# Kernel optimization log

Hardware: AMD Instinct MI355X
Metric: run time of the kernel (lower is better)

Reference implementation:

```python
import math
import jax, jax.numpy as jnp
import numpy as np

INPUT_SIZE = 256
HIDDEN_SIZE = 512
HISTORY_SIZE = 2048
SEQ_LEN = 512
BATCH = 256


def setup_inputs() -> dict:
    key = jax.random.key(0)
    ks = jax.random.split(key, 7)
    s = 0.05
    return {
        "x": jax.random.normal(ks[0], (SEQ_LEN, BATCH, INPUT_SIZE), jnp.float32),
        "hidden": jax.random.normal(ks[1], (1, BATCH, HIDDEN_SIZE), jnp.float32),
        "external": jax.random.normal(ks[2], (HISTORY_SIZE, INPUT_SIZE), jnp.float32),
        # GRU params (bias=False): weight_ih [3H, D_in], weight_hh [3H, H]
        "w_ih": jax.random.normal(ks[3], (3 * HIDDEN_SIZE, INPUT_SIZE), jnp.float32) * s,
        "w_hh": jax.random.normal(ks[4], (3 * HIDDEN_SIZE, HIDDEN_SIZE), jnp.float32) * s,
        "w_alpha": jax.random.normal(ks[5], (HISTORY_SIZE, HIDDEN_SIZE), jnp.float32) * s,
        "w_sigma": jax.random.normal(ks[6], (INPUT_SIZE, HIDDEN_SIZE), jnp.float32) * s,
    }


def reference(x, hidden, external, w_ih, w_hh, w_alpha, w_sigma):
    # --- GRU over the sequence (torch gate order: r, z, n) ---
    def gru_step(h, xt):
        gi = xt @ w_ih.T          # [B, 3H]
        gh = h @ w_hh.T           # [B, 3H]
        i_r, i_z, i_n = jnp.split(gi, 3, axis=-1)
        h_r, h_z, h_n = jnp.split(gh, 3, axis=-1)
        r = jax.nn.sigmoid(i_r + h_r)
        z = jax.nn.sigmoid(i_z + h_z)
        n = jnp.tanh(i_n + r * h_n)
        h_new = (1.0 - z) * n + z * h
        return h_new, None

    h_final, _ = jax.lax.scan(gru_step, hidden[0], x)   # [B, H]
    h_final = h_final[None]                              # [1, B, H]

    # Attention weights over history entries and predicted scale
    alpha = jax.nn.softmax(h_final @ w_alpha.T, axis=-1)  # [1, B, history]
    sigma = jnp.exp(h_final @ w_sigma.T)                  # [1, B, D]
    mu = alpha @ external                                 # [1, B, D]

    # Gaussian log-prob with diagonal factor L = diag(sigma) (M = L L^T)
    diff = x - mu                                         # [S, B, D]
    maha = jnp.sum(jnp.square(diff / sigma), axis=-1)     # [S, B]
    log_det = jnp.sum(jnp.log(jnp.abs(sigma)), axis=-1)   # [1, B]
    D = x.shape[-1]
    log2pi = np.float32(np.log(2.0 * np.pi))
    return -0.5 * (maha + D * log2pi) - log_det           # [S, B]
```

## Files before the change

kernel.cpp:

```cpp
#include <hip/hip_runtime.h>
#include <math.h>

#define BATCH 256
#define HID   512
#define DIN   256
#define SEQ   512
#define HIST  2048
#define NBLK  256
#define NGRP  8
#define GB    32

typedef __attribute__((ext_vector_type(8))) short short8;
typedef __attribute__((ext_vector_type(4))) float floatx4;
typedef __attribute__((ext_vector_type(8))) float floatx8;
typedef unsigned long long ull;
typedef unsigned int uint;

__device__ __forceinline__ unsigned short f32_bf16_rtne(float f) {
    uint u = __builtin_bit_cast(uint, f);
    uint r = u + 0x7FFFu + ((u >> 16) & 1u);
    return (unsigned short)(r >> 16);
}
__device__ __forceinline__ float bf16_f32(unsigned short s) {
    uint u = ((uint)s) << 16;
    return __builtin_bit_cast(float, u);
}
__device__ __forceinline__ float sigmoidf_(float v) {
    return 1.0f / (1.0f + __expf(-v));
}

__device__ __forceinline__ int h_widx(int b_local, int u) {
    return ((u >> 5) * 2 + (b_local >> 4)) * 512 +
           ((u >> 3) & 3) * 128 + (b_local & 15) * 8 + (u & 7);
}

__device__ __forceinline__ void lds_barrier() {
    __builtin_amdgcn_sched_barrier(0);
    asm volatile("s_waitcnt lgkmcnt(0)" ::: "memory");
    __builtin_amdgcn_s_barrier();
    __builtin_amdgcn_sched_barrier(0);
}

__global__ __launch_bounds__(256) void split_kernel(
    const float* __restrict__ src, short* __restrict__ hi, short* __restrict__ lo, int n)
{
    int i = blockIdx.x * 256 + threadIdx.x;
    if (i < n) {
        float v = src[i];
        unsigned short h = f32_bf16_rtne(v);
        hi[i] = (short)h;
        lo[i] = (short)f32_bf16_rtne(v - bf16_f32(h));
    }
}

__global__ __launch_bounds__(256) void pack_h_init(
    const float* __restrict__ hidden, uint* __restrict__ hp0)
{
    int i = blockIdx.x * 256 + threadIdx.x;
    int b = i >> 9, u = i & 511;
    int g = b >> 5, bl = b & 31;
    float v = hidden[i];
    unsigned short hi = f32_bf16_rtne(v);
    unsigned short lo = f32_bf16_rtne(v - bf16_f32(hi));
    lo = (unsigned short)(lo & 0xFFFCu);
    hp0[(size_t)g * 16384 + h_widx(bl, u)] = (uint)hi | ((uint)lo << 16);
}

__global__ __launch_bounds__(512, 2) void gru_persistent(
    const float* __restrict__ x,
    const float* __restrict__ hidden,
    uint* __restrict__ hpA, uint* __restrict__ hpB,
    const short* __restrict__ wih_hi, const short* __restrict__ wih_lo,
    const short* __restrict__ whh_hi, const short* __restrict__ whh_lo)
{
    const int bid  = blockIdx.x;
    const int g    = bid & 7;
    const int ublk = bid >> 3;
    const int u0   = ublk * 16;
    const int tid  = threadIdx.x;
    const int w    = tid >> 6;
    const int lane = tid & 63;
    const int quad = lane >> 4;
    const int n16  = lane & 15;
    const int mbase = g * GB;

    short8 Bh[3][3], Bl[3][3];
    #pragma unroll
    for (int gt = 0; gt < 3; ++gt) {
        const int row = gt * HID + u0 + n16;
        Bh[gt][0] = *(const short8*)(wih_hi + (size_t)row * DIN + w * 32 + quad * 8);
        Bl[gt][0] = *(const short8*)(wih_lo + (size_t)row * DIN + w * 32 + quad * 8);
        #pragma unroll
        for (int s = 0; s < 2; ++s) {
            const int K0h = w * 64 + s * 32;
            Bh[gt][1 + s] = *(const short8*)(whh_hi + (size_t)row * HID + K0h + quad * 8);
            Bl[gt][1 + s] = *(const short8*)(whh_lo + (size_t)row * HID + K0h + quad * 8);
        }
    }

    const int ob = tid >> 4;
    const int ou = tid & 15;
    float hp = hidden[(size_t)(mbase + ob) * HID + (u0 + ou)];
    const int my_widx = h_widx(ob, u0 + ou);

    __shared__ float P8[8][2][4][16][20];

#define MFMA3(AH, AL, BH, BL, ACC)                                        \
    ACC = __builtin_amdgcn_mfma_f32_16x16x32_bf16(AH, BH, ACC, 0, 0, 0);  \
    ACC = __builtin_amdgcn_mfma_f32_16x16x32_bf16(AL, BH, ACC, 0, 0, 0);  \
    ACC = __builtin_amdgcn_mfma_f32_16x16x32_bf16(AH, BL, ACC, 0, 0, 0);

    for (int t = 0; t < SEQ; ++t) {
        const uint* hb = ((t & 1) ? hpB : hpA) + (size_t)g * 16384;
        uint*       hd = ((t & 1) ? hpA : hpB) + (size_t)g * 16384;
        const ull*  hb8 = (const ull*)hb;
        const uint  tg  = (uint)t & 3u;

        const float* xt = x + (size_t)t * BATCH * DIN;
        const floatx8 xv0 = *(const floatx8*)(xt + (size_t)(mbase + n16) * DIN + w * 32 + quad * 8);
        const floatx8 xv1 = *(const floatx8*)(xt + (size_t)(mbase + 16 + n16) * DIN + w * 32 + quad * 8);

        ull hv[2][2][4];
        #pragma unroll
        for (int s = 0; s < 2; ++s)
            #pragma unroll
            for (int mt = 0; mt < 2; ++mt) {
                const ull* base = hb8 + (size_t)(((2 * w + s) * 2 + mt) * 64 + lane) * 4;
                #pragma unroll
                for (int j2 = 0; j2 < 4; ++j2)
                    hv[s][mt][j2] = __hip_atomic_load(base + j2, __ATOMIC_RELAXED,
                                                      __HIP_MEMORY_SCOPE_AGENT);
            }
        __builtin_amdgcn_sched_barrier(0);

        floatx4 acc[2][4];
        #pragma unroll
        for (int mt = 0; mt < 2; ++mt)
            #pragma unroll
            for (int a = 0; a < 4; ++a)
                acc[mt][a] = (floatx4){0.f, 0.f, 0.f, 0.f};

        #pragma unroll
        for (int mt = 0; mt < 2; ++mt) {
            const floatx8 xv = mt ? xv1 : xv0;
            short8 Ah, Al;
            #pragma unroll
            for (int j = 0; j < 8; ++j) {
                const float v = xv[j];
                const unsigned short hbw = f32_bf16_rtne(v);
                Ah[j] = (short)hbw;
                Al[j] = (short)f32_bf16_rtne(v - bf16_f32(hbw));
            }
            MFMA3(Ah, Al, Bh[0][0], Bl[0][0], acc[mt][0])
            MFMA3(Ah, Al, Bh[1][0], Bl[1][0], acc[mt][1])
            MFMA3(Ah, Al, Bh[2][0], Bl[2][0], acc[mt][2])
        }

        {
            bool okk = true;
            #pragma unroll
            for (int s = 0; s < 2; ++s)
                #pragma unroll
                for (int mt = 0; mt < 2; ++mt)
                    #pragma unroll
                    for (int j2 = 0; j2 < 4; ++j2) {
                        const ull v = hv[s][mt][j2];
                        okk = okk && (((uint)(v >> 16) & 3u) == tg) &&
                                     (((uint)(v >> 48) & 3u) == tg);
                    }
            while (!__all(okk)) {
                __builtin_amdgcn_s_sleep(1);
                okk = true;
                #pragma unroll
                for (int s = 0; s < 2; ++s)
                    #pragma unroll
                    for (int mt = 0; mt < 2; ++mt) {
                        const ull* base = hb8 + (size_t)(((2 * w + s) * 2 + mt) * 64 + lane) * 4;
                        #pragma unroll
                        for (int j2 = 0; j2 < 4; ++j2) {
                            ull v = hv[s][mt][j2];
                            const bool stale = (((uint)(v >> 16) & 3u) != tg) ||
                                               (((uint)(v >> 48) & 3u) != tg);
                            if (stale) {
                                v = __hip_atomic_load(base + j2, __ATOMIC_RELAXED,
                                                      __HIP_MEMORY_SCOPE_AGENT);
                                hv[s][mt][j2] = v;
                            }
                            okk = okk && (((uint)(v >> 16) & 3u) == tg) &&
                                         (((uint)(v >> 48) & 3u) == tg);
                        }
                    }
            }
        }

        #pragma unroll
        for (int s = 0; s < 2; ++s)
            #pragma unroll
            for (int mt = 0; mt < 2; ++mt) {
                union { int i[8]; short8 s8[2]; } U;
                #pragma unroll
                for (int j2 = 0; j2 < 4; ++j2) {
                    const uint w0 = (uint)hv[s][mt][j2];
                    const uint w1 = (uint)(hv[s][mt][j2] >> 32);
                    U.i[j2]     = (int)((w0 & 0xFFFFu) | (w1 << 16));
                    U.i[4 + j2] = (int)((w0 >> 16) | (w1 & 0xFFFF0000u));
                }
                const short8 Ah = U.s8[0];
                const short8 Al = U.s8[1];
                MFMA3(Ah, Al, Bh[0][1 + s], Bl[0][1 + s], acc[mt][0])
                MFMA3(Ah, Al, Bh[1][1 + s], Bl[1][1 + s], acc[mt][1])
                MFMA3(Ah, Al, Bh[2][1 + s], Bl[2][1 + s], acc[mt][3])
            }
#undef MFMA3

        #pragma unroll
        for (int mt = 0; mt < 2; ++mt)
            #pragma unroll
            for (int a = 0; a < 4; ++a)
                *(floatx4*)&P8[w][mt][a][n16][quad * 4] = acc[mt][a];
        lds_barrier();

        float sR = 0.f, sZ = 0.f, sNI = 0.f, sNH = 0.f;
        {
            const int mt = ob >> 4, rw = ob & 15;
            #pragma unroll
            for (int r = 0; r < 8; ++r) {
                sR  += P8[r][mt][0][ou][rw];
                sZ  += P8[r][mt][1][ou][rw];
                sNI += P8[r][mt][2][ou][rw];
                sNH += P8[r][mt][3][ou][rw];
            }
        }

        {
            const float r = sigmoidf_(sR);
            const float z = sigmoidf_(sZ);
            const float n = tanhf(sNI + r * sNH);
            const float hn = (1.0f - z) * n + z * hp;
            hp = hn;
            const unsigned short hbi = f32_bf16_rtne(hn);
            unsigned short lbi = f32_bf16_rtne(hn - bf16_f32(hbi));
            lbi = (unsigned short)((lbi & 0xFFFCu) | ((uint)(t + 1) & 3u));
            const uint word = (uint)hbi | ((uint)lbi << 16);
            __hip_atomic_store(hd + my_widx, word, __ATOMIC_RELAXED,
                               __HIP_MEMORY_SCOPE_AGENT);
        }

        lds_barrier();
    }
}

__global__ __launch_bounds__(256) void attn_kernel(
    const uint* __restrict__ hpk,
    const float* __restrict__ external,
    const float* __restrict__ w_alpha,
    const float* __restrict__ w_sigma,
    float* __restrict__ mu,
    float* __restrict__ inv_sig,
    float* __restrict__ log_det)
{
    const int b = blockIdx.x;
    const int t = threadIdx.x;

    __shared__ float hs[HID];
    __shared__ float al[HIST];
    __shared__ float red[256];

    const int g = b >> 5, bl = b & 31;
    for (int k = t; k < HID; k += 256) {
        const uint wv = hpk[(size_t)g * 16384 + h_widx(bl, k)];
        hs[k] = bf16_f32((unsigned short)(wv & 0xFFFF)) +
                bf16_f32((unsigned short)(wv >> 16));
    }
    __syncthreads();

    const float4* hs4 = (const float4*)hs;

    float lg[8];
    #pragma unroll
    for (int i = 0; i < 8; ++i) {
        const int e = t + 256 * i;
        const float4* wr = (const float4*)(w_alpha + (size_t)e * HID);
        float acc = 0.f;
        #pragma unroll 4
        for (int k = 0; k < HID / 4; ++k) {
            const float4 w4 = wr[k];
            const float4 h4 = hs4[k];
            acc += w4.x * h4.x + w4.y * h4.y + w4.z * h4.z + w4.w * h4.w;
        }
        lg[i] = acc;
    }

    float m = lg[0];
    #pragma unroll
    for (int i = 1; i < 8; ++i) m = fmaxf(m, lg[i]);
    red[t] = m;
    __syncthreads();
    for (int off = 128; off > 0; off >>= 1) {
        if (t < off) red[t] = fmaxf(red[t], red[t + off]);
        __syncthreads();
    }
    m = red[0];
    __syncthreads();

    float s = 0.f;
    #pragma unroll
    for (int i = 0; i < 8; ++i) {
        const float v = __expf(lg[i] - m);
        al[t + 256 * i] = v;
        s += v;
    }
    red[t] = s;
    __syncthreads();
    for (int off = 128; off > 0; off >>= 1) {
        if (t < off) red[t] += red[t + off];
        __syncthreads();
    }
    s = red[0];
    const float inv_s = 1.0f / s;
    __syncthreads();

    const int d = t;
    float acc_mu = 0.f;
    #pragma unroll 8
    for (int e = 0; e < HIST; ++e) {
        acc_mu += al[e] * external[(size_t)e * DIN + d];
    }
    mu[(size_t)b * DIN + d] = acc_mu * inv_s;

    const float4* ws = (const float4*)(w_sigma + (size_t)d * HID);
    float sl = 0.f;
    #pragma unroll 4
    for (int k = 0; k < HID / 4; ++k) {
        const float4 w4 = ws[k];
        const float4 h4 = hs4[k];
        sl += w4.x * h4.x + w4.y * h4.y + w4.z * h4.z + w4.w * h4.w;
    }
    inv_sig[(size_t)b * DIN + d] = __expf(-sl);

    red[t] = sl;
    __syncthreads();
    for (int off = 128; off > 0; off >>= 1) {
        if (t < off) red[t] += red[t + off];
        __syncthreads();
    }
    if (t == 0) log_det[b] = red[0];
}

__global__ __launch_bounds__(256) void out_kernel(
    const float* __restrict__ x,
    const float* __restrict__ mu,
    const float* __restrict__ inv_sig,
    const float* __restrict__ log_det,
    float* __restrict__ out)
{
    const int s = blockIdx.x;
    const int b = threadIdx.x;
    const float4* xr = (const float4*)(x + ((size_t)s * BATCH + b) * DIN);
    const float4* mr = (const float4*)(mu + (size_t)b * DIN);
    const float4* ir = (const float4*)(inv_sig + (size_t)b * DIN);

    float maha = 0.f;
    #pragma unroll 8
    for (int k = 0; k < DIN / 4; ++k) {
        const float4 xv = xr[k];
        const float4 mv = mr[k];
        const float4 iv = ir[k];
        const float t0 = (xv.x - mv.x) * iv.x;
        const float t1 = (xv.y - mv.y) * iv.y;
        const float t2 = (xv.z - mv.z) * iv.z;
        const float t3 = (xv.w - mv.w) * iv.w;
        maha += t0 * t0 + t1 * t1 + t2 * t2 + t3 * t3;
    }
    const float LOG2PI = 1.8378770664093453f;
    out[(size_t)s * BATCH + b] = -0.5f * (maha + (float)DIN * LOG2PI) - log_det[b];
}

extern "C" void kernel_launch(void* const* d_in, const int* in_sizes, int n_in,
                              void* d_out, int out_size, void* d_ws, size_t ws_size,
                              hipStream_t stream)
{
    const float* x        = (const float*)d_in[0];
    const float* hidden   = (const float*)d_in[1];
    const float* external = (const float*)d_in[2];
    const float* w_ih     = (const float*)d_in[3];
    const float* w_hh     = (const float*)d_in[4];
    const float* w_alpha  = (const float*)d_in[5];
    const float* w_sigma  = (const float*)d_in[6];

    const int NH  = BATCH * HID;
    const int NIH = 3 * HID * DIN;
    const int NHH = 3 * HID * HID;

    char* p = (char*)d_ws;
    uint* hpA = (uint*)p;             p += (size_t)NH * 4;
    uint* hpB = (uint*)p;             p += (size_t)NH * 4;
    short* wih_hi = (short*)p;        p += (size_t)NIH * 2;
    short* wih_lo = (short*)p;        p += (size_t)NIH * 2;
    short* whh_hi = (short*)p;        p += (size_t)NHH * 2;
    short* whh_lo = (short*)p;        p += (size_t)NHH * 2;
    float* mu      = (float*)p;       p += (size_t)BATCH * DIN * 4;
    float* inv_sig = (float*)p;       p += (size_t)BATCH * DIN * 4;
    float* log_det = (float*)p;       p += (size_t)BATCH * 4;

    (void)hipMemsetAsync(hpB, 0, (size_t)NH * 4, stream);

    split_kernel<<<(NIH + 255) / 256, 256, 0, stream>>>(w_ih, wih_hi, wih_lo, NIH);
    split_kernel<<<(NHH + 255) / 256, 256, 0, stream>>>(w_hh, whh_hi, whh_lo, NHH);
    pack_h_init<<<(NH + 255) / 256, 256, 0, stream>>>(hidden, hpA);

    gru_persistent<<<dim3(NBLK), dim3(512), 0, stream>>>(
        x, hidden, hpA, hpB, wih_hi, wih_lo, whh_hi, whh_lo);

    attn_kernel<<<dim3(BATCH), dim3(256), 0, stream>>>(
        hpA, external, w_alpha, w_sigma, mu, inv_sig, log_det);

    out_kernel<<<dim3(SEQ), dim3(256), 0, stream>>>(
        x, mu, inv_sig, log_det, (float*)d_out);
}
```

Before: 3.051 ms.

## Split GRU batch into 16 groups of 16, double-buffer LDS partials, prefetch x

```diff
diff --git a/kernel.cpp b/kernel.cpp
--- a/kernel.cpp
+++ b/kernel.cpp
@@ -6,9 +6,9 @@
 #define DIN   256
 #define SEQ   512
 #define HIST  2048
-#define NBLK  256
-#define NGRP  8
-#define GB    32
+#define NBLK  512
+#define NGRP  16
+#define GB    16
 
 typedef __attribute__((ext_vector_type(8))) short short8;
 typedef __attribute__((ext_vector_type(4))) float floatx4;
@@ -25,13 +25,16 @@
     uint u = ((uint)s) << 16;
     return __builtin_bit_cast(float, u);
 }
-__device__ __forceinline__ float sigmoidf_(float v) {
-    return 1.0f / (1.0f + __expf(-v));
+__device__ __forceinline__ float fsig(float v) {
+    return __fdividef(1.0f, 1.0f + __expf(-v));
+}
+__device__ __forceinline__ float ftanh(float v) {
+    const float e = __expf(2.0f * v);
+    return 1.0f - __fdividef(2.0f, e + 1.0f);
 }
 
 __device__ __forceinline__ int h_widx(int b_local, int u) {
-    return ((u >> 5) * 2 + (b_local >> 4)) * 512 +
-           ((u >> 3) & 3) * 128 + (b_local & 15) * 8 + (u & 7);
+    return (u >> 5) * 512 + ((u >> 3) & 3) * 128 + b_local * 8 + (u & 7);
 }
 
 __device__ __forceinline__ void lds_barrier() {
@@ -58,15 +61,15 @@
 {
     int i = blockIdx.x * 256 + threadIdx.x;
     int b = i >> 9, u = i & 511;
-    int g = b >> 5, bl = b & 31;
+    int g = b >> 4, bl = b & 15;
     float v = hidden[i];
     unsigned short hi = f32_bf16_rtne(v);
     unsigned short lo = f32_bf16_rtne(v - bf16_f32(hi));
     lo = (unsigned short)(lo & 0xFFFCu);
-    hp0[(size_t)g * 16384 + h_widx(bl, u)] = (uint)hi | ((uint)lo << 16);
-}
-
-__global__ __launch_bounds__(512, 2) void gru_persistent(
+    hp0[(size_t)g * 8192 + h_widx(bl, u)] = (uint)hi | ((uint)lo << 16);
+}
+
+__global__ __launch_bounds__(512, 4) void gru_persistent(
     const float* __restrict__ x,
     const float* __restrict__ hidden,
     uint* __restrict__ hpA, uint* __restrict__ hpB,
@@ -74,8 +77,8 @@
     const short* __restrict__ whh_hi, const short* __restrict__ whh_lo)
 {
     const int bid  = blockIdx.x;
-    const int g    = bid & 7;
-    const int ublk = bid >> 3;
+    const int g    = bid & 15;
+    const int ublk = bid >> 4;
     const int u0   = ublk * 16;
     const int tid  = threadIdx.x;
     const int w    = tid >> 6;
@@ -98,12 +101,14 @@
         }
     }
 
-    const int ob = tid >> 4;
+    const int ob = (tid >> 4) & 15;
     const int ou = tid & 15;
     float hp = hidden[(size_t)(mbase + ob) * HID + (u0 + ou)];
     const int my_widx = h_widx(ob, u0 + ou);
 
-    __shared__ float P8[8][2][4][16][20];
+    __shared__ float P[2][8][4][16][18];
+
+    floatx8 xv = *(const floatx8*)(x + (size_t)(mbase + n16) * DIN + w * 32 + quad * 8);
 
 #define MFMA3(AH, AL, BH, BL, ACC)                                        \
     ACC = __builtin_amdgcn_mfma_f32_16x16x32_bf16(AH, BH, ACC, 0, 0, 0);  \
@@ -111,38 +116,29 @@
     ACC = __builtin_amdgcn_mfma_f32_16x16x32_bf16(AH, BL, ACC, 0, 0, 0);
 
     for (int t = 0; t < SEQ; ++t) {
-        const uint* hb = ((t & 1) ? hpB : hpA) + (size_t)g * 16384;
-        uint*       hd = ((t & 1) ? hpA : hpB) + (size_t)g * 16384;
-        const ull*  hb8 = (const ull*)hb;
+        const uint* hbp = ((t & 1) ? hpB : hpA) + (size_t)g * 8192;
+        uint*       hdp = ((t & 1) ? hpA : hpB) + (size_t)g * 8192;
+        const ull*  hb8 = (const ull*)hbp;
         const uint  tg  = (uint)t & 3u;
-
-        const float* xt = x + (size_t)t * BATCH * DIN;
-        const floatx8 xv0 = *(const floatx8*)(xt + (size_t)(mbase + n16) * DIN + w * 32 + quad * 8);
-        const floatx8 xv1 = *(const floatx8*)(xt + (size_t)(mbase + 16 + n16) * DIN + w * 32 + quad * 8);
-
-        ull hv[2][2][4];
+        const int   p   = t & 1;
+
+        ull hv[2][4];
         #pragma unroll
-        for (int s = 0; s < 2; ++s)
+        for (int s = 0; s < 2; ++s) {
+            const ull* base = hb8 + (size_t)((2 * w + s) * 256 + quad * 64 + n16 * 4);
             #pragma unroll
-            for (int mt = 0; mt < 2; ++mt) {
-                const ull* base = hb8 + (size_t)(((2 * w + s) * 2 + mt) * 64 + lane) * 4;
-                #pragma unroll
-                for (int j2 = 0; j2 < 4; ++j2)
-                    hv[s][mt][j2] = __hip_atomic_load(base + j2, __ATOMIC_RELAXED,
-                                                      __HIP_MEMORY_SCOPE_AGENT);
-            }
+            for (int j2 = 0; j2 < 4; ++j2)
+                hv[s][j2] = __hip_atomic_load(base + j2, __ATOMIC_RELAXED,
+                                              __HIP_MEMORY_SCOPE_AGENT);
+        }
         __builtin_amdgcn_sched_barrier(0);
 
-        floatx4 acc[2][4];
+        floatx4 acc[4];
         #pragma unroll
-        for (int mt = 0; mt < 2; ++mt)
-            #pragma unroll
-            for (int a = 0; a < 4; ++a)
-                acc[mt][a] = (floatx4){0.f, 0.f, 0.f, 0.f};
-
-        #pragma unroll
-        for (int mt = 0; mt < 2; ++mt) {
-            const floatx8 xv = mt ? xv1 : xv0;
+        for (int a = 0; a < 4; ++a)
+            acc[a] = (floatx4){0.f, 0.f, 0.f, 0.f};
+
+        {
             short8 Ah, Al;
             #pragma unroll
             for (int j = 0; j < 8; ++j) {
@@ -151,9 +147,9 @@
                 Ah[j] = (short)hbw;
                 Al[j] = (short)f32_bf16_rtne(v - bf16_f32(hbw));
             }
-            MFMA3(Ah, Al, Bh[0][0], Bl[0][0], acc[mt][0])
-            MFMA3(Ah, Al, Bh[1][0], Bl[1][0], acc[mt][1])
-            MFMA3(Ah, Al, Bh[2][0], Bl[2][0], acc[mt][2])
+            MFMA3(Ah, Al, Bh[0][0], Bl[0][0], acc[0])
+            MFMA3(Ah, Al, Bh[1][0], Bl[1][0], acc[1])
+            MFMA3(Ah, Al, Bh[2][0], Bl[2][0], acc[2])
         }
 
         {
@@ -161,92 +157,83 @@
             #pragma unroll
             for (int s = 0; s < 2; ++s)
                 #pragma unroll
-                for (int mt = 0; mt < 2; ++mt)
-                    #pragma unroll
-                    for (int j2 = 0; j2 < 4; ++j2) {
-                        const ull v = hv[s][mt][j2];
-                        okk = okk && (((uint)(v >> 16) & 3u) == tg) &&
-                                     (((uint)(v >> 48) & 3u) == tg);
-                    }
+                for (int j2 = 0; j2 < 4; ++j2) {
+                    const ull v = hv[s][j2];
+                    okk = okk && (((uint)(v >> 16) & 3u) == tg) &&
+                                 (((uint)(v >> 48) & 3u) == tg);
+                }
             while (!__all(okk)) {
                 __builtin_amdgcn_s_sleep(1);
                 okk = true;
                 #pragma unroll
-                for (int s = 0; s < 2; ++s)
+                for (int s = 0; s < 2; ++s) {
+                    const ull* base = hb8 + (size_t)((2 * w + s) * 256 + quad * 64 + n16 * 4);
                     #pragma unroll
-                    for (int mt = 0; mt < 2; ++mt) {
-                        const ull* base = hb8 + (size_t)(((2 * w + s) * 2 + mt) * 64 + lane) * 4;
-                        #pragma unroll
-                        for (int j2 = 0; j2 < 4; ++j2) {
-                            ull v = hv[s][mt][j2];
-                            const bool stale = (((uint)(v >> 16) & 3u) != tg) ||
-                                               (((uint)(v >> 48) & 3u) != tg);
-                            if (stale) {
-                                v = __hip_atomic_load(base + j2, __ATOMIC_RELAXED,
-                                                      __HIP_MEMORY_SCOPE_AGENT);
-                                hv[s][mt][j2] = v;
-                            }
-                            okk = okk && (((uint)(v >> 16) & 3u) == tg) &&
-                                         (((uint)(v >> 48) & 3u) == tg);
+                    for (int j2 = 0; j2 < 4; ++j2) {
+                        ull v = hv[s][j2];
+                        const bool stale = (((uint)(v >> 16) & 3u) != tg) ||
+                                           (((uint)(v >> 48) & 3u) != tg);
+                        if (stale) {
+                            v = __hip_atomic_load(base + j2, __ATOMIC_RELAXED,
+                                                  __HIP_MEMORY_SCOPE_AGENT);
+                            hv[s][j2] = v;
                         }
+                        okk = okk && (((uint)(v >> 16) & 3u) == tg) &&
+                                     (((uint)(v >> 48) & 3u) == tg);
                     }
+                }
             }
         }
 
         #pragma unroll
-        for (int s = 0; s < 2; ++s)
+        for (int s = 0; s < 2; ++s) {
+            union { int i[8]; short8 s8[2]; } U;
             #pragma unroll
-            for (int mt = 0; mt < 2; ++mt) {
-                union { int i[8]; short8 s8[2]; } U;
-                #pragma unroll
-                for (int j2 = 0; j2 < 4; ++j2) {
-                    const uint w0 = (uint)hv[s][mt][j2];
-                    const uint w1 = (uint)(hv[s][mt][j2] >> 32);
-                    U.i[j2]     = (int)((w0 & 0xFFFFu) | (w1 << 16));
-                    U.i[4 + j2] = (int)((w0 >> 16) | (w1 & 0xFFFF0000u));
-                }
-                const short8 Ah = U.s8[0];
-                const short8 Al = U.s8[1];
-                MFMA3(Ah, Al, Bh[0][1 + s], Bl[0][1 + s], acc[mt][0])
-                MFMA3(Ah, Al, Bh[1][1 + s], Bl[1][1 + s], acc[mt][1])
-                MFMA3(Ah, Al, Bh[2][1 + s], Bl[2][1 + s], acc[mt][3])
+            for (int j2 = 0; j2 < 4; ++j2) {
+                const uint w0 = (uint)hv[s][j2];
+                const uint w1 = (uint)(hv[s][j2] >> 32);
+                U.i[j2]     = (int)((w0 & 0xFFFFu) | (w1 << 16));
+                U.i[4 + j2] = (int)((w0 >> 16) | (w1 & 0xFFFF0000u));
             }
+            const short8 Ah = U.s8[0];
+            const short8 Al = U.s8[1];
+            MFMA3(Ah, Al, Bh[0][1 + s], Bl[0][1 + s], acc[0])
+            MFMA3(Ah, Al, Bh[1][1 + s], Bl[1][1 + s], acc[1])
+            MFMA3(Ah, Al, Bh[2][1 + s], Bl[2][1 + s], acc[3])
+        }
 #undef MFMA3
 
         #pragma unroll
-        for (int mt = 0; mt < 2; ++mt)
-            #pragma unroll
-            for (int a = 0; a < 4; ++a)
-                *(floatx4*)&P8[w][mt][a][n16][quad * 4] = acc[mt][a];
+        for (int a = 0; a < 4; ++a)
+            *(floatx4*)&P[p][w][a][n16][quad * 4] = acc[a];
+
+        if (t + 1 < SEQ)
+            xv = *(const floatx8*)(x + ((size_t)(t + 1) * BATCH + mbase + n16) * DIN
+                                   + w * 32 + quad * 8);
+
         lds_barrier();
 
-        float sR = 0.f, sZ = 0.f, sNI = 0.f, sNH = 0.f;
-        {
-            const int mt = ob >> 4, rw = ob & 15;
+        if (tid < 256) {
+            float sR = 0.f, sZ = 0.f, sNI = 0.f, sNH = 0.f;
             #pragma unroll
             for (int r = 0; r < 8; ++r) {
-                sR  += P8[r][mt][0][ou][rw];
-                sZ  += P8[r][mt][1][ou][rw];
-                sNI += P8[r][mt][2][ou][rw];
-                sNH += P8[r][mt][3][ou][rw];
+                sR  += P[p][r][0][ou][ob];
+                sZ  += P[p][r][1][ou][ob];
+                sNI += P[p][r][2][ou][ob];
+                sNH += P[p][r][3][ou][ob];
             }
-        }
-
-        {
-            const float r = sigmoidf_(sR);
-            const float z = sigmoidf_(sZ);
-            const float n = tanhf(sNI + r * sNH);
+            const float rr = fsig(sR);
+            const float z  = fsig(sZ);
+            const float n  = ftanh(sNI + rr * sNH);
             const float hn = (1.0f - z) * n + z * hp;
             hp = hn;
             const unsigned short hbi = f32_bf16_rtne(hn);
             unsigned short lbi = f32_bf16_rtne(hn - bf16_f32(hbi));
             lbi = (unsigned short)((lbi & 0xFFFCu) | ((uint)(t + 1) & 3u));
             const uint word = (uint)hbi | ((uint)lbi << 16);
-            __hip_atomic_store(hd + my_widx, word, __ATOMIC_RELAXED,
+            __hip_atomic_store(hdp + my_widx, word, __ATOMIC_RELAXED,
                                __HIP_MEMORY_SCOPE_AGENT);
         }
-
-        lds_barrier();
     }
 }
 
@@ -266,9 +253,9 @@
     __shared__ float al[HIST];
     __shared__ float red[256];
 
-    const int g = b >> 5, bl = b & 31;
+    const int g = b >> 4, bl = b & 15;
     for (int k = t; k < HID; k += 256) {
-        const uint wv = hpk[(size_t)g * 16384 + h_widx(bl, k)];
+        const uint wv = hpk[(size_t)g * 8192 + h_widx(bl, k)];
         hs[k] = bf16_f32((unsigned short)(wv & 0xFFFF)) +
                 bf16_f32((unsigned short)(wv >> 16));
     }
```

Result: slower. 5.673 ms (+85.9%).

## Double-buffer partial-sum LDS, prefetch next x, and use fast gate math

Applied to the files above, without the earlier changes.

```diff
diff --git a/kernel.cpp b/kernel.cpp
--- a/kernel.cpp
+++ b/kernel.cpp
@@ -25,8 +25,12 @@
     uint u = ((uint)s) << 16;
     return __builtin_bit_cast(float, u);
 }
-__device__ __forceinline__ float sigmoidf_(float v) {
-    return 1.0f / (1.0f + __expf(-v));
+__device__ __forceinline__ float fsig(float v) {
+    return __fdividef(1.0f, 1.0f + __expf(-v));
+}
+__device__ __forceinline__ float ftanh(float v) {
+    const float e = __expf(2.0f * v);
+    return 1.0f - __fdividef(2.0f, e + 1.0f);
 }
 
 __device__ __forceinline__ int h_widx(int b_local, int u) {
@@ -103,7 +107,10 @@
     float hp = hidden[(size_t)(mbase + ob) * HID + (u0 + ou)];
     const int my_widx = h_widx(ob, u0 + ou);
 
-    __shared__ float P8[8][2][4][16][20];
+    __shared__ float P[2][8][2][4][16][18];
+
+    floatx8 xv0 = *(const floatx8*)(x + (size_t)(mbase + n16) * DIN + w * 32 + quad * 8);
+    floatx8 xv1 = *(const floatx8*)(x + (size_t)(mbase + 16 + n16) * DIN + w * 32 + quad * 8);
 
 #define MFMA3(AH, AL, BH, BL, ACC)                                        \
     ACC = __builtin_amdgcn_mfma_f32_16x16x32_bf16(AH, BH, ACC, 0, 0, 0);  \
@@ -111,14 +118,11 @@
     ACC = __builtin_amdgcn_mfma_f32_16x16x32_bf16(AH, BL, ACC, 0, 0, 0);
 
     for (int t = 0; t < SEQ; ++t) {
-        const uint* hb = ((t & 1) ? hpB : hpA) + (size_t)g * 16384;
-        uint*       hd = ((t & 1) ? hpA : hpB) + (size_t)g * 16384;
-        const ull*  hb8 = (const ull*)hb;
+        const uint* hbp = ((t & 1) ? hpB : hpA) + (size_t)g * 16384;
+        uint*       hdp = ((t & 1) ? hpA : hpB) + (size_t)g * 16384;
+        const ull*  hb8 = (const ull*)hbp;
         const uint  tg  = (uint)t & 3u;
-
-        const float* xt = x + (size_t)t * BATCH * DIN;
-        const floatx8 xv0 = *(const floatx8*)(xt + (size_t)(mbase + n16) * DIN + w * 32 + quad * 8);
-        const floatx8 xv1 = *(const floatx8*)(xt + (size_t)(mbase + 16 + n16) * DIN + w * 32 + quad * 8);
+        const int   p   = t & 1;
 
         ull hv[2][2][4];
         #pragma unroll
@@ -154,6 +158,12 @@
             MFMA3(Ah, Al, Bh[0][0], Bl[0][0], acc[mt][0])
             MFMA3(Ah, Al, Bh[1][0], Bl[1][0], acc[mt][1])
             MFMA3(Ah, Al, Bh[2][0], Bl[2][0], acc[mt][2])
+        }
+
+        if (t + 1 < SEQ) {
+            const float* xn = x + (size_t)(t + 1) * BATCH * DIN;
+            xv0 = *(const floatx8*)(xn + (size_t)(mbase + n16) * DIN + w * 32 + quad * 8);
+            xv1 = *(const floatx8*)(xn + (size_t)(mbase + 16 + n16) * DIN + w * 32 + quad * 8);
         }
 
         {
@@ -217,36 +227,32 @@
         for (int mt = 0; mt < 2; ++mt)
             #pragma unroll
             for (int a = 0; a < 4; ++a)
-                *(floatx4*)&P8[w][mt][a][n16][quad * 4] = acc[mt][a];
+                *(floatx4*)&P[p][w][mt][a][n16][quad * 4] = acc[mt][a];
+
         lds_barrier();
 
-        float sR = 0.f, sZ = 0.f, sNI = 0.f, sNH = 0.f;
         {
             const int mt = ob >> 4, rw = ob & 15;
+            float sR = 0.f, sZ = 0.f, sNI = 0.f, sNH = 0.f;
             #pragma unroll
             for (int r = 0; r < 8; ++r) {
-                sR  += P8[r][mt][0][ou][rw];
-                sZ  += P8[r][mt][1][ou][rw];
-                sNI += P8[r][mt][2][ou][rw];
-                sNH += P8[r][mt][3][ou][rw];
+                sR  += P[p][r][mt][0][ou][rw];
+                sZ  += P[p][r][mt][1][ou][rw];
+                sNI += P[p][r][mt][2][ou][rw];
+                sNH += P[p][r][mt][3][ou][rw];
             }
-        }
-
-        {
-            const float r = sigmoidf_(sR);
-            const float z = sigmoidf_(sZ);
-            const float n = tanhf(sNI + r * sNH);
+            const float rr = fsig(sR);
+            const float z  = fsig(sZ);
+            const float n  = ftanh(sNI + rr * sNH);
             const float hn = (1.0f - z) * n + z * hp;
             hp = hn;
             const unsigned short hbi = f32_bf16_rtne(hn);
             unsigned short lbi = f32_bf16_rtne(hn - bf16_f32(hbi));
             lbi = (unsigned short)((lbi & 0xFFFCu) | ((uint)(t + 1) & 3u));
             const uint word = (uint)hbi | ((uint)lbi << 16);
-            __hip_atomic_store(hd + my_widx, word, __ATOMIC_RELAXED,
+            __hip_atomic_store(hdp + my_widx, word, __ATOMIC_RELAXED,
                                __HIP_MEMORY_SCOPE_AGENT);
         }
-
-        lds_barrier();
     }
 }
 
```

Measured after the change: 4.803 ms. 1.57x slower.
